# Optimization experiments

Measured on AMD Instinct MI355X. Metric: run time of the kernel, lower is better.

Reference implementation:

```python
import jax, jax.numpy as jnp
import numpy as np

MIN_EXPERT_CAPACITY = 4
EPS = 1e-9
CAPACITY_FACTOR = 2.0  # eval capacity factor


def cumsum_exclusive(t, axis):
    return jnp.cumsum(t, axis=axis) - t


def safe_one_hot(idx, depth):
    # one_hot with an extra slot so idx == depth maps to nothing, then slice
    return jax.nn.one_hot(idx, depth + 1)[..., :depth]


def setup_inputs() -> dict:
    key = jax.random.key(0)
    k_x, k_g, k_w1, k_w2 = jax.random.split(key, 4)
    b, n, d, e, h = 2, 4096, 512, 16, 2048
    x = jax.random.normal(k_x, (b, n, d), dtype=jnp.float32)
    w_gating = jax.random.normal(k_g, (d, e), dtype=jnp.float32) / np.sqrt(d)
    w1 = jax.random.normal(k_w1, (e, d, h), dtype=jnp.float32) / np.sqrt(d)
    w2 = jax.random.normal(k_w2, (e, h, d), dtype=jnp.float32) / np.sqrt(h)
    return {"x": x, "w_gating": w_gating, "w1": w1, "w2": w2}


def top2_gating(x, w_gating):
    b, n, d = x.shape
    e = w_gating.shape[-1]
    raw_gates = jax.nn.softmax(jnp.einsum('bnd,de->bne', x, w_gating), axis=-1)

    gate_1 = jnp.max(raw_gates, axis=-1)
    index_1 = jnp.argmax(raw_gates, axis=-1)
    mask_1 = jax.nn.one_hot(index_1, e, dtype=raw_gates.dtype)

    gates_without_top1 = raw_gates * (1.0 - mask_1)
    gate_2 = jnp.max(gates_without_top1, axis=-1)
    index_2 = jnp.argmax(gates_without_top1, axis=-1)
    mask_2 = jax.nn.one_hot(index_2, e, dtype=raw_gates.dtype)

    denom = gate_1 + gate_2 + EPS
    gate_1 = gate_1 / denom
    gate_2 = gate_2 / denom

    # load-balancing loss
    density_1 = jnp.mean(mask_1, axis=-2)
    density_1_proxy = jnp.mean(raw_gates, axis=-2)
    loss = jnp.mean(density_1_proxy * density_1) * float(e * e)

    # second policy == 'all' -> keep mask_2 as-is

    capacity = max(min(n, int((n * 2) * CAPACITY_FACTOR / e)), MIN_EXPERT_CAPACITY)
    cap_f = float(capacity)

    pos1 = cumsum_exclusive(mask_1, axis=-2) * mask_1  # [b,n,e]
    mask_1 = mask_1 * (pos1 < cap_f).astype(mask_1.dtype)
    mask_1_count = jnp.sum(mask_1, axis=-2, keepdims=True)
    mask_1_flat = jnp.sum(mask_1, axis=-1)  # [b,n]
    pos1 = jnp.sum(pos1, axis=-1)
    gate_1 = gate_1 * mask_1_flat

    pos2 = (cumsum_exclusive(mask_2, axis=-2) + mask_1_count) * mask_2
    mask_2 = mask_2 * (pos2 < cap_f).astype(mask_2.dtype)
    mask_2_flat = jnp.sum(mask_2, axis=-1)
    pos2 = jnp.sum(pos2, axis=-1)
    gate_2 = gate_2 * mask_2_flat

    # combine tensor: [b, n, e, c]
    combine = (gate_1[..., None, None] * mask_1_flat[..., None, None]
               * jax.nn.one_hot(index_1, e, dtype=x.dtype)[..., None]
               * safe_one_hot(pos1.astype(jnp.int32), capacity)[..., None, :]
               + gate_2[..., None, None] * mask_2_flat[..., None, None]
               * jax.nn.one_hot(index_2, e, dtype=x.dtype)[..., None]
               * safe_one_hot(pos2.astype(jnp.int32), capacity)[..., None, :])
    dispatch = (combine > 0).astype(combine.dtype)
    return dispatch, combine, loss


def reference(x, w_gating, w1, w2):
    dispatch, combine, loss = top2_gating(x, w_gating)
    # dispatch: gather tokens into expert buckets [e, b, c, d]
    expert_inputs = jnp.einsum('bnd,bnec->ebcd', x, dispatch)
    # expert FFN (eval mode: dropout is identity)
    hidden = jax.nn.relu(jnp.einsum('ebcd,edh->ebch', expert_inputs, w1))
    expert_outputs = jnp.einsum('ebch,ehd->ebcd', hidden, w2)
    # combine back to token order, weighted by gate values
    output = jnp.einsum('ebcd,bnec->bnd', expert_outputs, combine)
    return output
```

## Files before the change

### kernel.cpp

```cpp
#include <hip/hip_runtime.h>

#define BB 2
#define NN 4096
#define DD 512
#define EE 16
#define HH 2048
#define CAP 1024
#define NTOK (BB*NN)
#define MM (BB*CAP)
#define MAXSTRIP 160

typedef unsigned short ushort_t;
typedef __attribute__((ext_vector_type(8))) short bf16x8;
typedef __attribute__((ext_vector_type(4))) float floatx4;

__device__ __forceinline__ ushort_t f2bf(float f) {
    union { float f; unsigned u; } v; v.f = f;
    unsigned r = v.u + 0x7fffu + ((v.u >> 16) & 1u);
    return (ushort_t)(r >> 16);
}

__device__ __forceinline__ void cp16(const void* g, void* l) {
    __builtin_amdgcn_global_load_lds(
        (const __attribute__((address_space(1))) void*)g,
        (__attribute__((address_space(3))) void*)l, 16, 0, 0);
}

__launch_bounds__(256)
__global__ void gating_kernel(const float* __restrict__ x,
                              const float* __restrict__ wg,
                              int* __restrict__ e1, int* __restrict__ e2,
                              float* __restrict__ g1, float* __restrict__ g2,
                              ushort_t* __restrict__ xbf) {
    int wave = threadIdx.x >> 6;
    int lane = threadIdx.x & 63;
    int t = blockIdx.x * 4 + wave;
    const float* xp = x + (size_t)t * DD;

    float4 xa = ((const float4*)xp)[lane * 2];
    float4 xb = ((const float4*)xp)[lane * 2 + 1];
    float xs[8] = {xa.x, xa.y, xa.z, xa.w, xb.x, xb.y, xb.z, xb.w};

    ushort4 h0, h1;
    h0.x = f2bf(xs[0]); h0.y = f2bf(xs[1]); h0.z = f2bf(xs[2]); h0.w = f2bf(xs[3]);
    h1.x = f2bf(xs[4]); h1.y = f2bf(xs[5]); h1.z = f2bf(xs[6]); h1.w = f2bf(xs[7]);
    ushort4* xo = (ushort4*)(xbf + (size_t)t * DD);
    xo[lane * 2] = h0; xo[lane * 2 + 1] = h1;

    float acc[EE];
#pragma unroll
    for (int e = 0; e < EE; e++) acc[e] = 0.f;
    int d0 = lane * 8;
#pragma unroll
    for (int j = 0; j < 8; j++) {
        const float* wrow = wg + (d0 + j) * EE;
#pragma unroll
        for (int e = 0; e < EE; e++) acc[e] = fmaf(xs[j], wrow[e], acc[e]);
    }
#pragma unroll
    for (int off = 32; off > 0; off >>= 1) {
#pragma unroll
        for (int e = 0; e < EE; e++) acc[e] += __shfl_xor(acc[e], off, 64);
    }
    if (lane == 0) {
        float m = acc[0];
#pragma unroll
        for (int e = 1; e < EE; e++) m = fmaxf(m, acc[e]);
        float p[EE]; float s = 0.f;
#pragma unroll
        for (int e = 0; e < EE; e++) { p[e] = __expf(acc[e] - m); s += p[e]; }
        float inv = 1.f / s;
#pragma unroll
        for (int e = 0; e < EE; e++) p[e] *= inv;
        int i1 = 0; float v1 = p[0];
#pragma unroll
        for (int e = 1; e < EE; e++) if (p[e] > v1) { v1 = p[e]; i1 = e; }
        int i2 = (i1 == 0) ? 1 : 0; float v2 = p[i2];
#pragma unroll
        for (int e = 0; e < EE; e++)
            if (e != i1 && p[e] > v2) { v2 = p[e]; i2 = e; }
        float denom = v1 + v2 + 1e-9f;
        e1[t] = i1; e2[t] = i2;
        g1[t] = v1 / denom; g2[t] = v2 / denom;
    }
}

__launch_bounds__(256)
__global__ void scan_kernel(const int* __restrict__ e1, const int* __restrict__ e2,
                            const float* __restrict__ g1, const float* __restrict__ g2,
                            int* __restrict__ s2t, float* __restrict__ s2g,
                            int* __restrict__ used) {
    int b = blockIdx.x / EE;
    int e = blockIdx.x % EE;
    int tid = threadIdx.x;
    const int base = b * NN;
    int n0 = tid * 16;

    unsigned m1 = 0, m2 = 0;
    int c1 = 0, c2 = 0;
#pragma unroll
    for (int j = 0; j < 16; j++) {
        int n = n0 + j;
        if (e1[base + n] == e) { m1 |= 1u << j; c1++; }
        if (e2[base + n] == e) { m2 |= 1u << j; c2++; }
    }
    __shared__ int s1[256], s2[256];
    __shared__ int s_used;
    s1[tid] = c1; s2[tid] = c2;
    __syncthreads();
    for (int off = 1; off < 256; off <<= 1) {
        int a1 = (tid >= off) ? s1[tid - off] : 0;
        int a2 = (tid >= off) ? s2[tid - off] : 0;
        __syncthreads();
        s1[tid] += a1; s2[tid] += a2;
        __syncthreads();
    }
    int total1 = s1[255];
    int total2 = s2[255];
    int kept1 = min(total1, CAP);
    int ex1 = s1[tid] - c1;
    int ex2 = s2[tid] - c2 + kept1;
    const int sbase = (e * BB + b) * CAP;
#pragma unroll
    for (int j = 0; j < 16; j++) {
        int n = n0 + j;
        if (m1 & (1u << j)) {
            if (ex1 < CAP) { s2t[sbase + ex1] = base + n; s2g[sbase + ex1] = g1[base + n]; }
            ex1++;
        }
        if (m2 & (1u << j)) {
            if (ex2 < CAP) { s2t[sbase + ex2] = base + n; s2g[sbase + ex2] = g2[base + n]; }
            ex2++;
        }
    }
    if (tid == 255) {
        int kept2 = min(total2, max(0, CAP - kept1));
        int u = kept1 + kept2;
        used[e * BB + b] = u;
        s_used = u;
    }
    __syncthreads();
    for (int i = s_used + tid; i < CAP; i += 256) s2t[sbase + i] = -1;
}

__global__ void worklist_kernel(const int* __restrict__ used, int* __restrict__ wl) {
    __shared__ int ns[32], pre[32];
    int i = threadIdx.x;
    if (i < 32) {
        int e = i >> 1, b = i & 1;
        ns[i] = (used[e * BB + b] + 127) >> 7;
    }
    __syncthreads();
    if (i == 0) {
        int acc = 0;
        for (int j = 0; j < 32; j++) { pre[j] = acc; acc += ns[j]; }
        wl[MAXSTRIP] = acc;
    }
    __syncthreads();
    if (i < 32) {
        int e = i >> 1, b = i & 1;
        int p = pre[i];
        for (int s = 0; s < ns[i]; s++)
            wl[p + s] = (e << 16) | (b * 8 + s);
    }
}

__global__ void transpose_bf16(const float* __restrict__ in,
                               ushort_t* __restrict__ outp, int R, int C) {
    __shared__ float tile[32][33];
    const float* slab = in + (size_t)blockIdx.z * R * C;
    ushort_t* oslab = outp + (size_t)blockIdx.z * R * C;
    int c0 = blockIdx.x * 32, r0 = blockIdx.y * 32;
    int tx = threadIdx.x, ty = threadIdx.y;
#pragma unroll
    for (int j = 0; j < 4; j++)
        tile[ty + j * 8][tx] = slab[(size_t)(r0 + ty + j * 8) * C + c0 + tx];
    __syncthreads();
#pragma unroll
    for (int j = 0; j < 4; j++)
        oslab[(size_t)(c0 + ty + j * 8) * R + r0 + tx] = f2bf(tile[tx][ty + j * 8]);
}

template <int MODE>
__launch_bounds__(256)
__global__ void gemm_mfma(const ushort_t* __restrict__ Abase,
                          const ushort_t* __restrict__ Bt,
                          void* __restrict__ Cout,
                          const int* __restrict__ wl,
                          const int* __restrict__ s2t,
                          const float* __restrict__ s2g) {
    constexpr int TN = (MODE == 0) ? 128 : 64;
    constexpr int K  = (MODE == 0) ? DD : HH;
    constexpr int KITERS = K / 32;
    constexpr int NV = (MODE == 0) ? 4 : 3;
    constexpr int MT = (MODE == 0) ? 4 : 2;

    int wi = blockIdx.y;
    if (wi >= wl[MAXSTRIP]) return;
    int entry = wl[wi];
    int e = entry >> 16;
    int ytile = entry & 0xffff;
    int col0 = blockIdx.x * TN;

    __shared__ ushort_t As[2][128 * 32];
    __shared__ ushort_t Bs[2][TN * 32];

    int tid = threadIdx.x;
    int lane = tid & 63;
    int wid = tid >> 6;
    int wave_m = (MODE == 0) ? ((wid & 1) << 6) : (wid << 5);
    int wave_n = (MODE == 0) ? ((wid >> 1) << 6) : 0;
    int lm = lane & 15;
    int quad = lane >> 4;
    int sw = (quad ^ ((lm >> 1) & 3)) * 8;

    const ushort_t* ga[2];
    const ushort_t* gb[NV - 2];
#pragma unroll
    for (int it = 0; it < 2; it++) {
        int idx = it * 256 + tid;
        int r = idx >> 2;
        int cg = (idx & 3) ^ ((r >> 1) & 3);
        if (MODE == 0) {
            int tok = s2t[e * MM + ytile * 128 + r];
            if (tok < 0) tok = 0;
            ga[it] = Abase + (size_t)tok * DD + cg * 8;
        } else {
            ga[it] = Abase + (size_t)(wi * 128 + r) * HH + cg * 8;
        }
    }
#pragma unroll
    for (int it = 0; it < NV - 2; it++) {
        int idx = it * 256 + tid;
        int r = idx >> 2;
        int cg = (idx & 3) ^ ((r >> 1) & 3);
        gb[it] = Bt + (size_t)e * HH * DD + (size_t)(col0 + r) * K + cg * 8;
    }

    auto stage = [&](int buf, int ki) {
#pragma unroll
        for (int it = 0; it < 2; it++)
            cp16(ga[it] + ki * 32, &As[buf][(it * 256 + tid) * 8]);
#pragma unroll
        for (int it = 0; it < NV - 2; it++)
            cp16(gb[it] + ki * 32, &Bs[buf][(it * 256 + tid) * 8]);
    };

    floatx4 acc[MT][4];
#pragma unroll
    for (int i = 0; i < MT; i++)
#pragma unroll
        for (int j = 0; j < 4; j++)
            acc[i][j] = (floatx4)(0.f);

    stage(0, 0);
#pragma unroll 2
    for (int ki = 0; ki < KITERS; ki++) {
        int cur = ki & 1;
        if (ki + 1 < KITERS) {
            stage(cur ^ 1, ki + 1);
            asm volatile("s_waitcnt vmcnt(%0)\ns_barrier" :: "i"(NV) : "memory");
        } else {
            asm volatile("s_waitcnt vmcnt(0)\ns_barrier" ::: "memory");
        }
        bf16x8 af[MT], bfr[4];
#pragma unroll
        for (int mt = 0; mt < MT; mt++)
            af[mt] = *(const bf16x8*)&As[cur][(wave_m + mt * 16 + lm) * 32 + sw];
#pragma unroll
        for (int nt = 0; nt < 4; nt++)
            bfr[nt] = *(const bf16x8*)&Bs[cur][(wave_n + nt * 16 + lm) * 32 + sw];
#pragma unroll
        for (int mt = 0; mt < MT; mt++)
#pragma unroll
            for (int nt = 0; nt < 4; nt++)
                acc[mt][nt] = __builtin_amdgcn_mfma_f32_16x16x32_bf16(
                    af[mt], bfr[nt], acc[mt][nt], 0, 0, 0);
        asm volatile("s_waitcnt lgkmcnt(0)\ns_barrier" ::: "memory");
    }

    if (MODE == 0) {
        ushort_t* hp = (ushort_t*)Cout + (size_t)wi * 128 * HH;
#pragma unroll
        for (int mt = 0; mt < MT; mt++) {
#pragma unroll
            for (int r = 0; r < 4; r++) {
                int row = wave_m + mt * 16 + quad * 4 + r;
#pragma unroll
                for (int nt = 0; nt < 4; nt++) {
                    int col = col0 + wave_n + nt * 16 + lm;
                    hp[(size_t)row * HH + col] = f2bf(fmaxf(acc[mt][nt][r], 0.f));
                }
            }
        }
    } else {
        float* outp = (float*)Cout;
#pragma unroll
        for (int mt = 0; mt < MT; mt++) {
#pragma unroll
            for (int r = 0; r < 4; r++) {
                int row = wave_m + mt * 16 + quad * 4 + r;
                int slot = e * MM + ytile * 128 + row;
                int tok = s2t[slot];
                if (tok < 0) continue;
                float g = s2g[slot];
#pragma unroll
                for (int nt = 0; nt < 4; nt++) {
                    int col = col0 + wave_n + nt * 16 + lm;
                    atomicAdd(outp + (size_t)tok * DD + col, g * acc[mt][nt][r]);
                }
            }
        }
    }
}

extern "C" void kernel_launch(void* const* d_in, const int* in_sizes, int n_in,
                              void* d_out, int out_size, void* d_ws, size_t ws_size,
                              hipStream_t stream) {
    const float* x  = (const float*)d_in[0];
    const float* wg = (const float*)d_in[1];
    const float* w1 = (const float*)d_in[2];
    const float* w2 = (const float*)d_in[3];
    float* out = (float*)d_out;

    char* ws = (char*)d_ws;
    int*      e1   = (int*)(ws);
    int*      e2   = (int*)(ws + 32768);
    float*    g1   = (float*)(ws + 65536);
    float*    g2   = (float*)(ws + 98304);
    int*      used = (int*)(ws + 131072);
    int*      wl   = (int*)(ws + 132096);
    int*      s2t  = (int*)(ws + 133120);
    float*    s2g  = (float*)(ws + 264192);
    ushort_t* xbf  = (ushort_t*)(ws + 395264);
    ushort_t* wt   = (ushort_t*)(ws + 8783872);
    ushort_t* hid  = (ushort_t*)(ws + 42338304);

    hipMemsetAsync(out, 0, (size_t)NTOK * DD * sizeof(float), stream);

    gating_kernel<<<NTOK / 4, 256, 0, stream>>>(x, wg, e1, e2, g1, g2, xbf);
    scan_kernel<<<BB * EE, 256, 0, stream>>>(e1, e2, g1, g2, s2t, s2g, used);
    worklist_kernel<<<1, 64, 0, stream>>>(used, wl);

    transpose_bf16<<<dim3(HH / 32, DD / 32, EE), dim3(32, 8), 0, stream>>>(w1, wt, DD, HH);
    gemm_mfma<0><<<dim3(HH / 128, MAXSTRIP), 256, 0, stream>>>(xbf, wt, hid, wl, s2t, s2g);

    transpose_bf16<<<dim3(DD / 32, HH / 32, EE), dim3(32, 8), 0, stream>>>(w2, wt, HH, DD);
    gemm_mfma<1><<<dim3(DD / 64, MAXSTRIP), 256, 0, stream>>>(hid, wt, out, wl, s2t, s2g);
}
```

Measured before the change: 394.4 us.

## Schedule GEMM tiles per XCD by expert and unify tiles to 128x128

```diff
diff --git a/kernel.cpp b/kernel.cpp
--- a/kernel.cpp
+++ b/kernel.cpp
@@ -143,7 +143,7 @@
     for (int i = s_used + tid; i < CAP; i += 256) s2t[sbase + i] = -1;
 }
 
-__global__ void worklist_kernel(const int* __restrict__ used, int* __restrict__ wl) {
+__global__ void schedule_kernel(const int* __restrict__ used, int* __restrict__ meta) {
     __shared__ int ns[32], pre[32];
     int i = threadIdx.x;
     if (i < 32) {
@@ -154,14 +154,35 @@
     if (i == 0) {
         int acc = 0;
         for (int j = 0; j < 32; j++) { pre[j] = acc; acc += ns[j]; }
-        wl[MAXSTRIP] = acc;
-    }
-    __syncthreads();
-    if (i < 32) {
-        int e = i >> 1, b = i & 1;
-        int p = pre[i];
-        for (int s = 0; s < ns[i]; s++)
-            wl[p + s] = (e << 16) | (b * 8 + s);
+    }
+    __syncthreads();
+    if (i < 16) {
+        int e = i;
+        int xcd = e & 7;
+        int mine  = ns[2 * e] + ns[2 * e + 1];
+        int po    = (e < 8) ? (e + 8) : (e - 8);
+        int other = ns[2 * po] + ns[2 * po + 1];
+        if (e < 8) {
+            meta[xcd]     = (mine + other) * 16;
+            meta[8 + xcd] = (mine + other) * 4;
+        }
+        int off = (e < 8) ? 0 : other;
+        int* sc1 = meta + 16 + xcd * 512 + off * 16;
+        int j = 0;
+        for (int col = 0; col < 16; col++)
+            for (int bb = 0; bb < 2; bb++)
+                for (int s = 0; s < ns[2 * e + bb]; s++) {
+                    int wi = pre[2 * e + bb] + s;
+                    sc1[j++] = (e << 17) | (wi << 9) | ((bb * 8 + s) << 5) | col;
+                }
+        int* sc2 = meta + 16 + 4096 + xcd * 128 + off * 4;
+        j = 0;
+        for (int col = 0; col < 4; col++)
+            for (int bb = 0; bb < 2; bb++)
+                for (int s = 0; s < ns[2 * e + bb]; s++) {
+                    int wi = pre[2 * e + bb] + s;
+                    sc2[j++] = (e << 17) | (wi << 9) | ((bb * 8 + s) << 5) | col;
+                }
     }
 }
 
@@ -186,36 +207,34 @@
 __global__ void gemm_mfma(const ushort_t* __restrict__ Abase,
                           const ushort_t* __restrict__ Bt,
                           void* __restrict__ Cout,
-                          const int* __restrict__ wl,
+                          const int* __restrict__ meta,
                           const int* __restrict__ s2t,
                           const float* __restrict__ s2g) {
-    constexpr int TN = (MODE == 0) ? 128 : 64;
-    constexpr int K  = (MODE == 0) ? DD : HH;
+    constexpr int K = (MODE == 0) ? DD : HH;
     constexpr int KITERS = K / 32;
-    constexpr int NV = (MODE == 0) ? 4 : 3;
-    constexpr int MT = (MODE == 0) ? 4 : 2;
-
-    int wi = blockIdx.y;
-    if (wi >= wl[MAXSTRIP]) return;
-    int entry = wl[wi];
-    int e = entry >> 16;
-    int ytile = entry & 0xffff;
-    int col0 = blockIdx.x * TN;
+
+    int xcd = blockIdx.x;
+    if ((int)blockIdx.y >= meta[(MODE == 0 ? 0 : 8) + xcd]) return;
+    int job = meta[16 + (MODE == 0 ? 0 : 4096) + xcd * (MODE == 0 ? 512 : 128) + blockIdx.y];
+    int col0  = (job & 31) * 128;
+    int ytile = (job >> 5) & 15;
+    int wi    = (job >> 9) & 255;
+    int e     = job >> 17;
 
     __shared__ ushort_t As[2][128 * 32];
-    __shared__ ushort_t Bs[2][TN * 32];
+    __shared__ ushort_t Bs[2][128 * 32];
 
     int tid = threadIdx.x;
     int lane = tid & 63;
     int wid = tid >> 6;
-    int wave_m = (MODE == 0) ? ((wid & 1) << 6) : (wid << 5);
-    int wave_n = (MODE == 0) ? ((wid >> 1) << 6) : 0;
+    int wave_m = (wid & 1) << 6;
+    int wave_n = (wid >> 1) << 6;
     int lm = lane & 15;
     int quad = lane >> 4;
     int sw = (quad ^ ((lm >> 1) & 3)) * 8;
 
     const ushort_t* ga[2];
-    const ushort_t* gb[NV - 2];
+    const ushort_t* gb[2];
 #pragma unroll
     for (int it = 0; it < 2; it++) {
         int idx = it * 256 + tid;
@@ -228,12 +247,6 @@
         } else {
             ga[it] = Abase + (size_t)(wi * 128 + r) * HH + cg * 8;
         }
-    }
-#pragma unroll
-    for (int it = 0; it < NV - 2; it++) {
-        int idx = it * 256 + tid;
-        int r = idx >> 2;
-        int cg = (idx & 3) ^ ((r >> 1) & 3);
         gb[it] = Bt + (size_t)e * HH * DD + (size_t)(col0 + r) * K + cg * 8;
     }
 
@@ -242,13 +255,13 @@
         for (int it = 0; it < 2; it++)
             cp16(ga[it] + ki * 32, &As[buf][(it * 256 + tid) * 8]);
 #pragma unroll
-        for (int it = 0; it < NV - 2; it++)
+        for (int it = 0; it < 2; it++)
             cp16(gb[it] + ki * 32, &Bs[buf][(it * 256 + tid) * 8]);
     };
 
-    floatx4 acc[MT][4];
-#pragma unroll
-    for (int i = 0; i < MT; i++)
+    floatx4 acc[4][4];
+#pragma unroll
+    for (int i = 0; i < 4; i++)
 #pragma unroll
         for (int j = 0; j < 4; j++)
             acc[i][j] = (floatx4)(0.f);
@@ -259,19 +272,19 @@
         int cur = ki & 1;
         if (ki + 1 < KITERS) {
             stage(cur ^ 1, ki + 1);
-            asm volatile("s_waitcnt vmcnt(%0)\ns_barrier" :: "i"(NV) : "memory");
+            asm volatile("s_waitcnt vmcnt(4)\ns_barrier" ::: "memory");
         } else {
             asm volatile("s_waitcnt vmcnt(0)\ns_barrier" ::: "memory");
         }
-        bf16x8 af[MT], bfr[4];
-#pragma unroll
-        for (int mt = 0; mt < MT; mt++)
+        bf16x8 af[4], bfr[4];
+#pragma unroll
+        for (int mt = 0; mt < 4; mt++)
             af[mt] = *(const bf16x8*)&As[cur][(wave_m + mt * 16 + lm) * 32 + sw];
 #pragma unroll
         for (int nt = 0; nt < 4; nt++)
             bfr[nt] = *(const bf16x8*)&Bs[cur][(wave_n + nt * 16 + lm) * 32 + sw];
 #pragma unroll
-        for (int mt = 0; mt < MT; mt++)
+        for (int mt = 0; mt < 4; mt++)
 #pragma unroll
             for (int nt = 0; nt < 4; nt++)
                 acc[mt][nt] = __builtin_amdgcn_mfma_f32_16x16x32_bf16(
@@ -282,7 +295,7 @@
     if (MODE == 0) {
         ushort_t* hp = (ushort_t*)Cout + (size_t)wi * 128 * HH;
 #pragma unroll
-        for (int mt = 0; mt < MT; mt++) {
+        for (int mt = 0; mt < 4; mt++) {
 #pragma unroll
             for (int r = 0; r < 4; r++) {
                 int row = wave_m + mt * 16 + quad * 4 + r;
@@ -296,7 +309,7 @@
     } else {
         float* outp = (float*)Cout;
 #pragma unroll
-        for (int mt = 0; mt < MT; mt++) {
+        for (int mt = 0; mt < 4; mt++) {
 #pragma unroll
             for (int r = 0; r < 4; r++) {
                 int row = wave_m + mt * 16 + quad * 4 + r;
@@ -329,22 +342,22 @@
     float*    g1   = (float*)(ws + 65536);
     float*    g2   = (float*)(ws + 98304);
     int*      used = (int*)(ws + 131072);
-    int*      wl   = (int*)(ws + 132096);
-    int*      s2t  = (int*)(ws + 133120);
-    float*    s2g  = (float*)(ws + 264192);
-    ushort_t* xbf  = (ushort_t*)(ws + 395264);
-    ushort_t* wt   = (ushort_t*)(ws + 8783872);
-    ushort_t* hid  = (ushort_t*)(ws + 42338304);
+    int*      meta = (int*)(ws + 132096);
+    int*      s2t  = (int*)(ws + 152704);
+    float*    s2g  = (float*)(ws + 283776);
+    ushort_t* xbf  = (ushort_t*)(ws + 414848);
+    ushort_t* wt   = (ushort_t*)(ws + 8803456);
+    ushort_t* hid  = (ushort_t*)(ws + 42357888);
 
     hipMemsetAsync(out, 0, (size_t)NTOK * DD * sizeof(float), stream);
 
     gating_kernel<<<NTOK / 4, 256, 0, stream>>>(x, wg, e1, e2, g1, g2, xbf);
     scan_kernel<<<BB * EE, 256, 0, stream>>>(e1, e2, g1, g2, s2t, s2g, used);
-    worklist_kernel<<<1, 64, 0, stream>>>(used, wl);
+    schedule_kernel<<<1, 64, 0, stream>>>(used, meta);
 
     transpose_bf16<<<dim3(HH / 32, DD / 32, EE), dim3(32, 8), 0, stream>>>(w1, wt, DD, HH);
-    gemm_mfma<0><<<dim3(HH / 128, MAXSTRIP), 256, 0, stream>>>(xbf, wt, hid, wl, s2t, s2g);
+    gemm_mfma<0><<<dim3(8, 512), 256, 0, stream>>>(xbf, wt, hid, meta, s2t, s2g);
 
     transpose_bf16<<<dim3(DD / 32, HH / 32, EE), dim3(32, 8), 0, stream>>>(w2, wt, HH, DD);
-    gemm_mfma<1><<<dim3(DD / 64, MAXSTRIP), 256, 0, stream>>>(hid, wt, out, wl, s2t, s2g);
-}
+    gemm_mfma<1><<<dim3(8, 128), 256, 0, stream>>>(hid, wt, out, meta, s2t, s2g);
+}
```

New measurement: 366.6 us. 1.08x faster.
